# Performance work log

Measured on AMD Instinct MI355X. Metric: run time of the kernel, lower is better.

Reference implementation:

```python
import jax, jax.numpy as jnp
import numpy as np

N_NODES = 100000
N_EDGES = 600000
F_IN, HID = 128, 128


def _gcn_conv(x, edge_index, W, b):
    """PyG-style GCNConv: add self-loops, symmetric deg^-1/2 normalization,
    linear transform, scatter-add aggregation at target nodes."""
    n = x.shape[0]
    loop = jnp.arange(n, dtype=edge_index.dtype)
    src = jnp.concatenate([edge_index[0], loop])
    dst = jnp.concatenate([edge_index[1], loop])
    deg = jax.ops.segment_sum(jnp.ones_like(dst, dtype=x.dtype), dst, num_segments=n)
    dinv = jnp.where(deg > 0, jax.lax.rsqrt(deg), 0.0)
    norm = dinv[src] * dinv[dst]                      # [E+N]
    xw = x @ W                                        # [N, out]
    msg = xw[src] * norm[:, None]                     # gather + scale
    out = jax.ops.segment_sum(msg, dst, num_segments=n)
    return out + b


def setup_inputs() -> dict:
    key = jax.random.key(0)
    ks = jax.random.split(key, 10)
    x = jax.random.normal(ks[0], (N_NODES, F_IN), dtype=jnp.float32)
    edge_index = jax.random.randint(ks[1], (2, N_EDGES), 0, N_NODES, dtype=jnp.int64)
    s = lambda fi: 1.0 / np.sqrt(fi)
    W1 = jax.random.normal(ks[2], (F_IN, HID), dtype=jnp.float32) * s(F_IN)
    b1 = jnp.zeros((HID,), dtype=jnp.float32)
    W2 = jax.random.normal(ks[3], (HID, HID // 2), dtype=jnp.float32) * s(HID)
    b2 = jnp.zeros((HID // 2,), dtype=jnp.float32)
    Wh1 = jax.random.normal(ks[4], (HID // 2, 16), dtype=jnp.float32) * s(HID // 2)
    bh1 = jnp.zeros((16,), dtype=jnp.float32)
    Wh2 = jax.random.normal(ks[5], (16, 1), dtype=jnp.float32) * s(16)
    bh2 = jnp.zeros((1,), dtype=jnp.float32)
    return {"x": x, "edge_index": edge_index, "W1": W1, "b1": b1,
            "W2": W2, "b2": b2, "Wh1": Wh1, "bh1": bh1, "Wh2": Wh2, "bh2": bh2}


def reference(x, edge_index, W1, b1, W2, b2, Wh1, bh1, Wh2, bh2):
    h = jax.nn.relu(_gcn_conv(x, edge_index, W1, b1))      # conv1 + relu
    # dropout: eval mode -> identity
    h = jax.nn.relu(_gcn_conv(h, edge_index, W2, b2))      # conv2 + relu
    h = jax.nn.gelu(h @ Wh1 + bh1, approximate=False)      # head linear + GELU
    out = jax.nn.sigmoid(h @ Wh2 + bh2)                    # linear + sigmoid
    return out[..., 0]                                     # squeeze(-1) -> [N]
```

## Files before the change

kernel.cpp:

```cpp
#include <hip/hip_runtime.h>
#include <hip/hip_bf16.h>
#include <math.h>

#define N_NODES 100000
#define N_EDGES 600000
#define F1 128
#define F2 64

#define DEG_BLOCKS   ((N_EDGES + 255) / 256)
#define CONVW_ELEMS  (128 * 128 + 128 * 64)
#define CONVW_BLOCKS ((CONVW_ELEMS + 255) / 256)
#define MG1_BLOCKS   ((N_NODES + 63) / 64)
#define GG_BLOCKS    (N_NODES / 16)
#define GH_BLOCKS    (N_NODES / 32)

typedef __attribute__((ext_vector_type(8))) short bf16x8;
typedef __attribute__((ext_vector_type(4))) float f32x4;

__device__ inline short bfbits(float x) {
    __hip_bfloat16 h = __float2bfloat16(x);
    return *reinterpret_cast<short*>(&h);
}
__device__ inline float bf2f(short u) {
    unsigned int x = ((unsigned int)(unsigned short)u) << 16;
    return __uint_as_float(x);
}


__global__ __launch_bounds__(256) void dc_kernel(const int* __restrict__ dst, int* __restrict__ deg,
                                                 int* __restrict__ rank,
                                                 const float* __restrict__ W1, const float* __restrict__ W2,
                                                 unsigned short* __restrict__ Wt1, unsigned short* __restrict__ Wt2) {
    if (blockIdx.x < DEG_BLOCKS) {
        int e = blockIdx.x * 256 + threadIdx.x;
        if (e < N_EDGES) rank[e] = atomicAdd(&deg[dst[e]], 1);
    } else {
        int i = (blockIdx.x - DEG_BLOCKS) * 256 + threadIdx.x;
        if (i < 128 * 128) {
            int k = i / 128, n = i % 128;
            Wt1[n * 128 + k] = (unsigned short)bfbits(W1[i]);
        } else if (i < CONVW_ELEMS) {
            int j = i - 128 * 128;
            int k = j / 64, n = j % 64;
            Wt2[n * 128 + k] = (unsigned short)bfbits(W2[j]);
        }
    }
}


__global__ void prep_kernel(const int* __restrict__ deg, int* __restrict__ counter,
                            float* __restrict__ dinv, int* __restrict__ off) {
    int i = blockIdx.x * blockDim.x + threadIdx.x;
    int d = (i < N_NODES) ? deg[i] : 0;
    if (i < N_NODES) dinv[i] = rsqrtf((float)(d + 1));
    int incl = d;
    #pragma unroll
    for (int o = 1; o < 64; o <<= 1) {
        int v = __shfl_up(incl, o);
        if ((threadIdx.x & 63) >= o) incl += v;
    }
    int base = 0;
    if ((threadIdx.x & 63) == 63) base = atomicAdd(counter, incl);
    base = __shfl(base, 63);
    if (i < N_NODES) off[i] = base + incl - d;
}


__global__ __launch_bounds__(256) void mf_kernel(const float* __restrict__ X,
                                                 const unsigned short* __restrict__ Wt,
                                                 const float* __restrict__ dinv,
                                                 unsigned short* __restrict__ out,
                                                 const int* __restrict__ src, const int* __restrict__ dst,
                                                 const int* __restrict__ rank, const int* __restrict__ off,
                                                 int* __restrict__ csr_src) {
    const int tid = threadIdx.x;
    if (blockIdx.x >= MG1_BLOCKS) {
        int e = (blockIdx.x - MG1_BLOCKS) * 256 + tid;
        if (e < N_EDGES) {
            int s = src[e], d = dst[e];
            int pos = off[d] + rank[e];
            csr_src[pos] = s;
        }
        return;
    }

    constexpr int NT = 128 / 16;
    const int wid = tid >> 6;
    const int l   = tid & 63;
    const int l16 = l & 15;
    const int kg  = l >> 4;

    const int row = blockIdx.x * 64 + wid * 16 + l16;
    const int rowc = (row < N_NODES) ? row : (N_NODES - 1);

    bf16x8 a[4];
    const float* xp = X + (size_t)rowc * 128 + kg * 8;
    #pragma unroll
    for (int ks = 0; ks < 4; ks++) {
        const float4 v0 = *(const float4*)(xp + ks * 32);
        const float4 v1 = *(const float4*)(xp + ks * 32 + 4);
        bf16x8 t;
        t[0] = bfbits(v0.x); t[1] = bfbits(v0.y); t[2] = bfbits(v0.z); t[3] = bfbits(v0.w);
        t[4] = bfbits(v1.x); t[5] = bfbits(v1.y); t[6] = bfbits(v1.z); t[7] = bfbits(v1.w);
        a[ks] = t;
    }

    f32x4 acc[NT];
    #pragma unroll
    for (int t = 0; t < NT; t++) acc[t] = (f32x4){0.f, 0.f, 0.f, 0.f};

    #pragma unroll
    for (int t = 0; t < NT; t++) {
        const unsigned short* wp = Wt + (size_t)(t * 16 + l16) * 128 + kg * 8;
        #pragma unroll
        for (int ks = 0; ks < 4; ks++) {
            bf16x8 bb = *(const bf16x8*)(wp + ks * 32);
            acc[t] = __builtin_amdgcn_mfma_f32_16x16x32_bf16(bb, a[ks], acc[t], 0, 0, 0);
        }
    }

    if (row < N_NODES) {
        const float dv = dinv[row];
        #pragma unroll
        for (int t = 0; t < NT; t++) {
            short4 pk;
            pk.x = bfbits(acc[t][0] * dv); pk.y = bfbits(acc[t][1] * dv);
            pk.z = bfbits(acc[t][2] * dv); pk.w = bfbits(acc[t][3] * dv);
            *(short4*)(out + (size_t)row * 128 + t * 16 + kg * 4) = pk;
        }
    }
}


__global__ __launch_bounds__(256) void gg_kernel(const unsigned short* __restrict__ xw,
                                                 const float* __restrict__ dinv,
                                                 const int* __restrict__ off,
                                                 const int* __restrict__ deg,
                                                 const int* __restrict__ csr_src,
                                                 const float* __restrict__ bias,
                                                 const unsigned short* __restrict__ Wt2,
                                                 unsigned short* __restrict__ xw2) {
    __shared__ unsigned short H[16 * 128];
    char* Hb = (char*)H;
    const int tid = threadIdx.x;
    const int nl = tid >> 4;
    const int c  = tid & 15;
    const int n  = blockIdx.x * 16 + nl;

    const float dn = dinv[n];
    float acc[8];
    {
        const bf16x8 v = *(const bf16x8*)(xw + (size_t)n * 128 + c * 8);
        #pragma unroll
        for (int i = 0; i < 8; i++) acc[i] = bf2f(v[i]);
    }
    const int e0 = off[n];
    const int e1 = e0 + deg[n];
    int sbuf[4];
    if (e0 < e1) {
        #pragma unroll
        for (int u = 0; u < 4; u++) {
            const int jj = e0 + u;
            sbuf[u] = csr_src[(jj < e1) ? jj : (e1 - 1)];
        }
    }
    for (int j = e0; j < e1; j += 4) {
        int s[4];
        #pragma unroll
        for (int u = 0; u < 4; u++) s[u] = sbuf[u];
        const int jn = j + 4;
        if (jn < e1) {
            #pragma unroll
            for (int u = 0; u < 4; u++) {
                const int jj = jn + u;
                sbuf[u] = csr_src[(jj < e1) ? jj : (e1 - 1)];
            }
        }
        float m[4]; bf16x8 v[4];
        #pragma unroll
        for (int u = 0; u < 4; u++) {
            m[u] = (j + u < e1) ? 1.f : 0.f;
            v[u] = *(const bf16x8*)(xw + (size_t)s[u] * 128 + c * 8);
        }
        #pragma unroll
        for (int u = 0; u < 4; u++) {
            #pragma unroll
            for (int i = 0; i < 8; i++) acc[i] += bf2f(v[u][i]) * m[u];
        }
    }
    bf16x8 o;
    #pragma unroll
    for (int i = 0; i < 8; i++) o[i] = bfbits(fmaxf(dn * acc[i] + bias[c * 8 + i], 0.f));
    *(bf16x8*)(Hb + nl * 256 + ((c * 16) ^ ((nl & 7) << 4))) = o;
    __syncthreads();

    const int w   = tid >> 6;
    const int l   = tid & 63;
    const int l16 = l & 15;
    const int kg  = l >> 4;
    bf16x8 a[4];
    #pragma unroll
    for (int ks = 0; ks < 4; ks++)
        a[ks] = *(const bf16x8*)(Hb + l16 * 256 + ((kg * 16 + ks * 64) ^ ((l16 & 7) << 4)));
    const unsigned short* wp = Wt2 + (size_t)(w * 16 + l16) * 128 + kg * 8;
    f32x4 acc2 = (f32x4){0.f, 0.f, 0.f, 0.f};
    #pragma unroll
    for (int ks = 0; ks < 4; ks++) {
        bf16x8 bb = *(const bf16x8*)(wp + ks * 32);
        acc2 = __builtin_amdgcn_mfma_f32_16x16x32_bf16(bb, a[ks], acc2, 0, 0, 0);
    }
    const int node = blockIdx.x * 16 + l16;
    const float dv = dinv[node];
    short4 pk;
    pk.x = bfbits(acc2[0] * dv); pk.y = bfbits(acc2[1] * dv);
    pk.z = bfbits(acc2[2] * dv); pk.w = bfbits(acc2[3] * dv);
    *(short4*)(xw2 + (size_t)node * 64 + w * 16 + kg * 4) = pk;
}


__global__ __launch_bounds__(256) void gh_kernel(const unsigned short* __restrict__ xw2,
                                                 const float* __restrict__ dinv,
                                                 const int* __restrict__ off,
                                                 const int* __restrict__ deg,
                                                 const int* __restrict__ csr_src,
                                                 const float* __restrict__ b2,
                                                 const float* __restrict__ Wh1,
                                                 const float* __restrict__ bh1,
                                                 const float* __restrict__ Wh2,
                                                 const float* __restrict__ bh2,
                                                 float* __restrict__ out) {
    __shared__ float h2s[32 * 68];
    __shared__ float W1s[64 * 16];
    __shared__ float W2s[16];
    __shared__ float b1s[16];
    const int tid = threadIdx.x;

    ((float4*)W1s)[tid] = ((const float4*)Wh1)[tid];
    if (tid < 16) { W2s[tid] = Wh2[tid]; b1s[tid] = bh1[tid]; }

    const int nl = tid >> 3;
    const int c  = tid & 7;
    const int n  = blockIdx.x * 32 + nl;

    const float dn = dinv[n];
    float acc[8];
    {
        const bf16x8 v = *(const bf16x8*)(xw2 + (size_t)n * 64 + c * 8);
        #pragma unroll
        for (int i = 0; i < 8; i++) acc[i] = bf2f(v[i]);
    }
    const int e0 = off[n];
    const int e1 = e0 + deg[n];
    int sbuf[4];
    if (e0 < e1) {
        #pragma unroll
        for (int u = 0; u < 4; u++) {
            const int jj = e0 + u;
            sbuf[u] = csr_src[(jj < e1) ? jj : (e1 - 1)];
        }
    }
    for (int j = e0; j < e1; j += 4) {
        int s[4];
        #pragma unroll
        for (int u = 0; u < 4; u++) s[u] = sbuf[u];
        const int jn = j + 4;
        if (jn < e1) {
            #pragma unroll
            for (int u = 0; u < 4; u++) {
                const int jj = jn + u;
                sbuf[u] = csr_src[(jj < e1) ? jj : (e1 - 1)];
            }
        }
        float m[4]; bf16x8 v[4];
        #pragma unroll
        for (int u = 0; u < 4; u++) {
            m[u] = (j + u < e1) ? 1.f : 0.f;
            v[u] = *(const bf16x8*)(xw2 + (size_t)s[u] * 64 + c * 8);
        }
        #pragma unroll
        for (int u = 0; u < 4; u++) {
            #pragma unroll
            for (int i = 0; i < 8; i++) acc[i] += bf2f(v[u][i]) * m[u];
        }
    }
    float4 f0, f1;
    f0.x = bf2f(bfbits(fmaxf(dn * acc[0] + b2[c * 8 + 0], 0.f)));
    f0.y = bf2f(bfbits(fmaxf(dn * acc[1] + b2[c * 8 + 1], 0.f)));
    f0.z = bf2f(bfbits(fmaxf(dn * acc[2] + b2[c * 8 + 2], 0.f)));
    f0.w = bf2f(bfbits(fmaxf(dn * acc[3] + b2[c * 8 + 3], 0.f)));
    f1.x = bf2f(bfbits(fmaxf(dn * acc[4] + b2[c * 8 + 4], 0.f)));
    f1.y = bf2f(bfbits(fmaxf(dn * acc[5] + b2[c * 8 + 5], 0.f)));
    f1.z = bf2f(bfbits(fmaxf(dn * acc[6] + b2[c * 8 + 6], 0.f)));
    f1.w = bf2f(bfbits(fmaxf(dn * acc[7] + b2[c * 8 + 7], 0.f)));
    *(float4*)&h2s[nl * 68 + c * 8]     = f0;
    *(float4*)&h2s[nl * 68 + c * 8 + 4] = f1;
    __syncthreads();

    const int l  = tid & 15;
    const int nn = tid >> 4;
    #pragma unroll
    for (int ss = 0; ss < 2; ss++) {
        const int node_l = ss * 16 + nn;
        float s = b1s[l];
        #pragma unroll 8
        for (int k = 0; k < 64; k++)
            s += h2s[node_l * 68 + k] * W1s[k * 16 + l];
        float g = 0.5f * s * (1.f + erff(s * 0.70710678118654752f));
        float p = g * W2s[l];
        p += __shfl_xor(p, 1);
        p += __shfl_xor(p, 2);
        p += __shfl_xor(p, 4);
        p += __shfl_xor(p, 8);
        if (l == 0) {
            const float z = p + bh2[0];
            out[blockIdx.x * 32 + node_l] = 1.f / (1.f + expf(-z));
        }
    }
}


extern "C" void kernel_launch(void* const* d_in, const int* in_sizes, int n_in,
                              void* d_out, int out_size, void* d_ws, size_t ws_size,
                              hipStream_t stream) {
    const float* x   = (const float*)d_in[0];
    const int*   ei  = (const int*)d_in[1];
    const float* W1  = (const float*)d_in[2];
    const float* b1  = (const float*)d_in[3];
    const float* W2  = (const float*)d_in[4];
    const float* b2  = (const float*)d_in[5];
    const float* Wh1 = (const float*)d_in[6];
    const float* bh1 = (const float*)d_in[7];
    const float* Wh2 = (const float*)d_in[8];
    const float* bh2 = (const float*)d_in[9];
    float* out = (float*)d_out;

    const int* srcA = ei;
    const int* dstA = ei + N_EDGES;

    char* ws = (char*)d_ws;
    const size_t MB = 1u << 20;
    float* dinv    = (float*)(ws);
    int*   deg     = (int*)  (ws + MB / 2);
    int*   counter = deg + N_NODES;
    int*   off     = (int*)  (ws + MB);
    int*   rank    = (int*)  (ws + MB + MB / 2);
    int*   csr_src = (int*)  (ws + 4 * MB);
    unsigned short* Wt1 = (unsigned short*)(ws + 7 * MB);
    unsigned short* Wt2 = Wt1 + 128 * 128;
    unsigned short* bufA = (unsigned short*)(ws + 8 * MB);
    unsigned short* xw2  = (unsigned short*)(ws + 34 * MB);

    hipMemsetAsync(deg, 0, (N_NODES + 1) * sizeof(int), stream);
    dc_kernel<<<DEG_BLOCKS + CONVW_BLOCKS, 256, 0, stream>>>(dstA, deg, rank, W1, W2, Wt1, Wt2);
    prep_kernel<<<(N_NODES + 255) / 256, 256, 0, stream>>>(deg, counter, dinv, off);
    mf_kernel<<<MG1_BLOCKS + DEG_BLOCKS, 256, 0, stream>>>(x, Wt1, dinv, bufA, srcA, dstA, rank, off, csr_src);

    gg_kernel<<<GG_BLOCKS, 256, 0, stream>>>(bufA, dinv, off, deg, csr_src, b1, Wt2, xw2);

    gh_kernel<<<GH_BLOCKS, 256, 0, stream>>>(xw2, dinv, off, deg, csr_src, b2,
                                             Wh1, bh1, Wh2, bh2, out);
}
```

Before: 154.7 us.

## Aggregate raw features before W1 and bucket CSR scatter by destination block

Layer 1 now aggregates dinv-scaled bf16 input features first and applies W1 afterwards, inside the gather kernel, with bias and ReLU applied after the matmul. This removes the standalone X@W1 MFMA pass and its write/read of an intermediate. The CSR build now goes through bucketed int2 staging plus a second pass, so the scattered writes to csr_src become localized. The software prefetch of source indices in both gather loops is dropped. In exchange the change adds a kernel launch, atomics on per-bucket tails and an extra staging buffer, and the reordered matmul changes bf16 rounding slightly.

```diff
diff --git a/kernel.cpp b/kernel.cpp
--- a/kernel.cpp
+++ b/kernel.cpp
@@ -10,7 +10,8 @@
 #define DEG_BLOCKS   ((N_EDGES + 255) / 256)
 #define CONVW_ELEMS  (128 * 128 + 128 * 64)
 #define CONVW_BLOCKS ((CONVW_ELEMS + 255) / 256)
-#define MG1_BLOCKS   ((N_NODES + 63) / 64)
+#define XB_BLOCKS    ((N_NODES * 128) / 2048)
+#define NBUCK        ((N_EDGES + 255) / 256)
 #define GG_BLOCKS    (N_NODES / 16)
 #define GH_BLOCKS    (N_NODES / 32)
 
@@ -66,82 +67,62 @@
 }
 
 
-__global__ __launch_bounds__(256) void mf_kernel(const float* __restrict__ X,
-                                                 const unsigned short* __restrict__ Wt,
+__global__ __launch_bounds__(256) void cf_kernel(const float* __restrict__ X,
                                                  const float* __restrict__ dinv,
-                                                 unsigned short* __restrict__ out,
+                                                 unsigned short* __restrict__ Xb,
                                                  const int* __restrict__ src, const int* __restrict__ dst,
                                                  const int* __restrict__ rank, const int* __restrict__ off,
-                                                 int* __restrict__ csr_src) {
+                                                 int* __restrict__ tails, int2* __restrict__ buck) {
     const int tid = threadIdx.x;
-    if (blockIdx.x >= MG1_BLOCKS) {
-        int e = (blockIdx.x - MG1_BLOCKS) * 256 + tid;
+    if (blockIdx.x < XB_BLOCKS) {
+        const size_t f = ((size_t)blockIdx.x * 256 + tid) * 8;
+        const int row = (int)(f >> 7);
+        const float dv = dinv[row];
+        const float4 v0 = *(const float4*)(X + f);
+        const float4 v1 = *(const float4*)(X + f + 4);
+        bf16x8 t;
+        t[0] = bfbits(v0.x * dv); t[1] = bfbits(v0.y * dv);
+        t[2] = bfbits(v0.z * dv); t[3] = bfbits(v0.w * dv);
+        t[4] = bfbits(v1.x * dv); t[5] = bfbits(v1.y * dv);
+        t[6] = bfbits(v1.z * dv); t[7] = bfbits(v1.w * dv);
+        *(bf16x8*)(Xb + f) = t;
+    } else {
+        int e = (blockIdx.x - XB_BLOCKS) * 256 + tid;
         if (e < N_EDGES) {
             int s = src[e], d = dst[e];
             int pos = off[d] + rank[e];
-            csr_src[pos] = s;
-        }
-        return;
-    }
-
-    constexpr int NT = 128 / 16;
-    const int wid = tid >> 6;
-    const int l   = tid & 63;
-    const int l16 = l & 15;
-    const int kg  = l >> 4;
-
-    const int row = blockIdx.x * 64 + wid * 16 + l16;
-    const int rowc = (row < N_NODES) ? row : (N_NODES - 1);
-
-    bf16x8 a[4];
-    const float* xp = X + (size_t)rowc * 128 + kg * 8;
-    #pragma unroll
-    for (int ks = 0; ks < 4; ks++) {
-        const float4 v0 = *(const float4*)(xp + ks * 32);
-        const float4 v1 = *(const float4*)(xp + ks * 32 + 4);
-        bf16x8 t;
-        t[0] = bfbits(v0.x); t[1] = bfbits(v0.y); t[2] = bfbits(v0.z); t[3] = bfbits(v0.w);
-        t[4] = bfbits(v1.x); t[5] = bfbits(v1.y); t[6] = bfbits(v1.z); t[7] = bfbits(v1.w);
-        a[ks] = t;
-    }
-
-    f32x4 acc[NT];
-    #pragma unroll
-    for (int t = 0; t < NT; t++) acc[t] = (f32x4){0.f, 0.f, 0.f, 0.f};
-
-    #pragma unroll
-    for (int t = 0; t < NT; t++) {
-        const unsigned short* wp = Wt + (size_t)(t * 16 + l16) * 128 + kg * 8;
-        #pragma unroll
-        for (int ks = 0; ks < 4; ks++) {
-            bf16x8 bb = *(const bf16x8*)(wp + ks * 32);
-            acc[t] = __builtin_amdgcn_mfma_f32_16x16x32_bf16(bb, a[ks], acc[t], 0, 0, 0);
-        }
-    }
-
-    if (row < N_NODES) {
-        const float dv = dinv[row];
-        #pragma unroll
-        for (int t = 0; t < NT; t++) {
-            short4 pk;
-            pk.x = bfbits(acc[t][0] * dv); pk.y = bfbits(acc[t][1] * dv);
-            pk.z = bfbits(acc[t][2] * dv); pk.w = bfbits(acc[t][3] * dv);
-            *(short4*)(out + (size_t)row * 128 + t * 16 + kg * 4) = pk;
-        }
-    }
-}
-
-
-__global__ __launch_bounds__(256) void gg_kernel(const unsigned short* __restrict__ xw,
+            int b = pos >> 8;
+            int slot = atomicAdd(&tails[b], 1);
+            buck[b * 256 + slot] = make_int2(s, pos);
+        }
+    }
+}
+
+
+__global__ __launch_bounds__(256) void p2_kernel(const int2* __restrict__ buck,
+                                                 int* __restrict__ csr_src) {
+    const int b = blockIdx.x;
+    const int cnt = min(256, N_EDGES - b * 256);
+    if (threadIdx.x < cnt) {
+        int2 v = buck[b * 256 + threadIdx.x];
+        csr_src[v.y] = v.x;
+    }
+}
+
+
+__global__ __launch_bounds__(256) void gg_kernel(const unsigned short* __restrict__ Xb,
                                                  const float* __restrict__ dinv,
                                                  const int* __restrict__ off,
                                                  const int* __restrict__ deg,
                                                  const int* __restrict__ csr_src,
-                                                 const float* __restrict__ bias,
+                                                 const float* __restrict__ b1,
+                                                 const unsigned short* __restrict__ Wt1,
                                                  const unsigned short* __restrict__ Wt2,
                                                  unsigned short* __restrict__ xw2) {
     __shared__ unsigned short H[16 * 128];
-    char* Hb = (char*)H;
+    __shared__ unsigned short H2[16 * 128];
+    char* Hb  = (char*)H;
+    char* H2b = (char*)H2;
     const int tid = threadIdx.x;
     const int nl = tid >> 4;
     const int c  = tid & 15;
@@ -150,37 +131,24 @@
     const float dn = dinv[n];
     float acc[8];
     {
-        const bf16x8 v = *(const bf16x8*)(xw + (size_t)n * 128 + c * 8);
+        const bf16x8 v = *(const bf16x8*)(Xb + (size_t)n * 128 + c * 8);
         #pragma unroll
         for (int i = 0; i < 8; i++) acc[i] = bf2f(v[i]);
     }
     const int e0 = off[n];
     const int e1 = e0 + deg[n];
-    int sbuf[4];
-    if (e0 < e1) {
-        #pragma unroll
-        for (int u = 0; u < 4; u++) {
-            const int jj = e0 + u;
-            sbuf[u] = csr_src[(jj < e1) ? jj : (e1 - 1)];
-        }
-    }
     for (int j = e0; j < e1; j += 4) {
         int s[4];
         #pragma unroll
-        for (int u = 0; u < 4; u++) s[u] = sbuf[u];
-        const int jn = j + 4;
-        if (jn < e1) {
-            #pragma unroll
-            for (int u = 0; u < 4; u++) {
-                const int jj = jn + u;
-                sbuf[u] = csr_src[(jj < e1) ? jj : (e1 - 1)];
-            }
+        for (int u = 0; u < 4; u++) {
+            const int jj = j + u;
+            s[u] = csr_src[(jj < e1) ? jj : (e1 - 1)];
         }
         float m[4]; bf16x8 v[4];
         #pragma unroll
         for (int u = 0; u < 4; u++) {
             m[u] = (j + u < e1) ? 1.f : 0.f;
-            v[u] = *(const bf16x8*)(xw + (size_t)s[u] * 128 + c * 8);
+            v[u] = *(const bf16x8*)(Xb + (size_t)s[u] * 128 + c * 8);
         }
         #pragma unroll
         for (int u = 0; u < 4; u++) {
@@ -188,10 +156,12 @@
             for (int i = 0; i < 8; i++) acc[i] += bf2f(v[u][i]) * m[u];
         }
     }
-    bf16x8 o;
-    #pragma unroll
-    for (int i = 0; i < 8; i++) o[i] = bfbits(fmaxf(dn * acc[i] + bias[c * 8 + i], 0.f));
-    *(bf16x8*)(Hb + nl * 256 + ((c * 16) ^ ((nl & 7) << 4))) = o;
+    {
+        bf16x8 o;
+        #pragma unroll
+        for (int i = 0; i < 8; i++) o[i] = bfbits(dn * acc[i]);
+        *(bf16x8*)(Hb + nl * 256 + ((c * 16) ^ ((nl & 7) << 4))) = o;
+    }
     __syncthreads();
 
     const int w   = tid >> 6;
@@ -202,18 +172,42 @@
     #pragma unroll
     for (int ks = 0; ks < 4; ks++)
         a[ks] = *(const bf16x8*)(Hb + l16 * 256 + ((kg * 16 + ks * 64) ^ ((l16 & 7) << 4)));
-    const unsigned short* wp = Wt2 + (size_t)(w * 16 + l16) * 128 + kg * 8;
-    f32x4 acc2 = (f32x4){0.f, 0.f, 0.f, 0.f};
+    #pragma unroll
+    for (int t = 0; t < 2; t++) {
+        const int colbase = w * 32 + t * 16;
+        const unsigned short* wp = Wt1 + (size_t)(colbase + l16) * 128 + kg * 8;
+        f32x4 acc2 = (f32x4){0.f, 0.f, 0.f, 0.f};
+        #pragma unroll
+        for (int ks = 0; ks < 4; ks++) {
+            bf16x8 bb = *(const bf16x8*)(wp + ks * 32);
+            acc2 = __builtin_amdgcn_mfma_f32_16x16x32_bf16(bb, a[ks], acc2, 0, 0, 0);
+        }
+        const int col0 = colbase + kg * 4;
+        short4 pk;
+        pk.x = bfbits(fmaxf(acc2[0] + b1[col0 + 0], 0.f));
+        pk.y = bfbits(fmaxf(acc2[1] + b1[col0 + 1], 0.f));
+        pk.z = bfbits(fmaxf(acc2[2] + b1[col0 + 2], 0.f));
+        pk.w = bfbits(fmaxf(acc2[3] + b1[col0 + 3], 0.f));
+        *(short4*)(H2b + l16 * 256 + ((col0 * 2) ^ ((l16 & 7) << 4))) = pk;
+    }
+    __syncthreads();
+
+    bf16x8 a2[4];
+    #pragma unroll
+    for (int ks = 0; ks < 4; ks++)
+        a2[ks] = *(const bf16x8*)(H2b + l16 * 256 + ((kg * 16 + ks * 64) ^ ((l16 & 7) << 4)));
+    const unsigned short* wp2 = Wt2 + (size_t)(w * 16 + l16) * 128 + kg * 8;
+    f32x4 acc3 = (f32x4){0.f, 0.f, 0.f, 0.f};
     #pragma unroll
     for (int ks = 0; ks < 4; ks++) {
-        bf16x8 bb = *(const bf16x8*)(wp + ks * 32);
-        acc2 = __builtin_amdgcn_mfma_f32_16x16x32_bf16(bb, a[ks], acc2, 0, 0, 0);
+        bf16x8 bb = *(const bf16x8*)(wp2 + ks * 32);
+        acc3 = __builtin_amdgcn_mfma_f32_16x16x32_bf16(bb, a2[ks], acc3, 0, 0, 0);
     }
     const int node = blockIdx.x * 16 + l16;
     const float dv = dinv[node];
     short4 pk;
-    pk.x = bfbits(acc2[0] * dv); pk.y = bfbits(acc2[1] * dv);
-    pk.z = bfbits(acc2[2] * dv); pk.w = bfbits(acc2[3] * dv);
+    pk.x = bfbits(acc3[0] * dv); pk.y = bfbits(acc3[1] * dv);
+    pk.z = bfbits(acc3[2] * dv); pk.w = bfbits(acc3[3] * dv);
     *(short4*)(xw2 + (size_t)node * 64 + w * 16 + kg * 4) = pk;
 }
 
@@ -251,25 +245,12 @@
     }
     const int e0 = off[n];
     const int e1 = e0 + deg[n];
-    int sbuf[4];
-    if (e0 < e1) {
-        #pragma unroll
-        for (int u = 0; u < 4; u++) {
-            const int jj = e0 + u;
-            sbuf[u] = csr_src[(jj < e1) ? jj : (e1 - 1)];
-        }
-    }
     for (int j = e0; j < e1; j += 4) {
         int s[4];
         #pragma unroll
-        for (int u = 0; u < 4; u++) s[u] = sbuf[u];
-        const int jn = j + 4;
-        if (jn < e1) {
-            #pragma unroll
-            for (int u = 0; u < 4; u++) {
-                const int jj = jn + u;
-                sbuf[u] = csr_src[(jj < e1) ? jj : (e1 - 1)];
-            }
+        for (int u = 0; u < 4; u++) {
+            const int jj = j + u;
+            s[u] = csr_src[(jj < e1) ? jj : (e1 - 1)];
         }
         float m[4]; bf16x8 v[4];
         #pragma unroll
@@ -342,20 +323,24 @@
     float* dinv    = (float*)(ws);
     int*   deg     = (int*)  (ws + MB / 2);
     int*   counter = deg + N_NODES;
+    int*   tails   = counter + 1;
     int*   off     = (int*)  (ws + MB);
     int*   rank    = (int*)  (ws + MB + MB / 2);
     int*   csr_src = (int*)  (ws + 4 * MB);
     unsigned short* Wt1 = (unsigned short*)(ws + 7 * MB);
     unsigned short* Wt2 = Wt1 + 128 * 128;
-    unsigned short* bufA = (unsigned short*)(ws + 8 * MB);
-    unsigned short* xw2  = (unsigned short*)(ws + 34 * MB);
-
-    hipMemsetAsync(deg, 0, (N_NODES + 1) * sizeof(int), stream);
+    unsigned short* Xb  = (unsigned short*)(ws + 8 * MB);
+    unsigned short* xw2 = (unsigned short*)(ws + 34 * MB);
+    int2*  buck    = (int2*) (ws + 47 * MB);
+
+    hipMemsetAsync(deg, 0, (N_NODES + 1 + NBUCK) * sizeof(int), stream);
     dc_kernel<<<DEG_BLOCKS + CONVW_BLOCKS, 256, 0, stream>>>(dstA, deg, rank, W1, W2, Wt1, Wt2);
     prep_kernel<<<(N_NODES + 255) / 256, 256, 0, stream>>>(deg, counter, dinv, off);
-    mf_kernel<<<MG1_BLOCKS + DEG_BLOCKS, 256, 0, stream>>>(x, Wt1, dinv, bufA, srcA, dstA, rank, off, csr_src);
-
-    gg_kernel<<<GG_BLOCKS, 256, 0, stream>>>(bufA, dinv, off, deg, csr_src, b1, Wt2, xw2);
+
+    cf_kernel<<<XB_BLOCKS + DEG_BLOCKS, 256, 0, stream>>>(x, dinv, Xb, srcA, dstA, rank, off, tails, buck);
+    p2_kernel<<<NBUCK, 256, 0, stream>>>(buck, csr_src);
+
+    gg_kernel<<<GG_BLOCKS, 256, 0, stream>>>(Xb, dinv, off, deg, csr_src, b1, Wt1, Wt2, xw2);
 
     gh_kernel<<<GH_BLOCKS, 256, 0, stream>>>(xw2, dinv, off, deg, csr_src, b2,
                                              Wh1, bh1, Wh2, bh2, out);
```

Result: slower. 216.5 us (+40.0%).
